# Kernel optimization log

Measured on AMD Instinct MI355X. Metric: run time of the kernel, lower is better.

## Reference

```python
import jax, jax.numpy as jnp
import numpy as np

N = 50000      # node_num
DIN = 128      # input_dim
DH = 128       # hidden_dim
DE = 128       # embedding_dim
DD = 128       # decoder_dim
NE = 800000    # num edges (before self loops)
B = 4096       # drug pairs
EPS = 1e-5


def setup_inputs() -> dict:
    key = jax.random.key(0)
    ks = jax.random.split(key, 16)
    x = jax.random.normal(ks[0], (N, DIN), jnp.float32)
    edge_index = jax.random.randint(ks[1], (2, NE), 0, N, dtype=jnp.int32)
    drug_index = jax.random.randint(ks[2], (B, 2), 0, N, dtype=jnp.int32)
    s = 0.05  # weight scale for numerical sanity
    return {
        "x": x,
        "edge_index": edge_index,
        "drug_index": drug_index,
        "w1": jax.random.normal(ks[3], (DIN, DH), jnp.float32) * s,
        "b1": jnp.zeros((DH,), jnp.float32),
        "w2": jax.random.normal(ks[4], (DH, DH), jnp.float32) * s,
        "b2": jnp.zeros((DH,), jnp.float32),
        "w3": jax.random.normal(ks[5], (DH, DE), jnp.float32) * s,
        "b3": jnp.zeros((DE,), jnp.float32),
        "g1": jnp.ones((DH,), jnp.float32), "be1": jnp.zeros((DH,), jnp.float32),
        "g2": jnp.ones((DH,), jnp.float32), "be2": jnp.zeros((DH,), jnp.float32),
        "g3": jnp.ones((DE,), jnp.float32), "be3": jnp.zeros((DE,), jnp.float32),
        "p1": jax.random.normal(ks[6], (DE, DD), jnp.float32) * s,
        "p2": jax.random.normal(ks[7], (DD, DD), jnp.float32) * s,
    }


def gcn_conv(x, row, col, W, b):
    # row/col already include self loops; PyG: message from row (source), aggregated at col (target)
    n = x.shape[0]
    h = x @ W + b                                   # linear first, as in GCNConv.forward
    deg = jnp.zeros((n,), h.dtype).at[col].add(1.0)  # degree(col) incl. self loops -> >= 1
    dis = deg ** -0.5
    norm = dis[row] * dis[col]                      # [E+N]
    msg = norm[:, None] * h[row]                    # [E+N, d] gather
    return jax.ops.segment_sum(msg, col, num_segments=n)  # scatter-add


def batch_norm(x, gamma, beta):
    m = jnp.mean(x, axis=0)
    v = jnp.mean((x - m) ** 2, axis=0)  # biased var, as torch BatchNorm training
    return (x - m) * jax.lax.rsqrt(v + EPS) * gamma + beta


def leaky(x):
    return jnp.where(x >= 0, x, 0.1 * x)  # LeakyReLU(0.1)


def reference(x, edge_index, drug_index, w1, b1, w2, b2, w3, b3,
              g1, be1, g2, be2, g3, be3, p1, p2):
    n = x.shape[0]
    self_loop = jnp.arange(n, dtype=edge_index.dtype)
    row = jnp.concatenate([edge_index[0], self_loop])
    col = jnp.concatenate([edge_index[1], self_loop])

    h = leaky(batch_norm(gcn_conv(x, row, col, w1, b1), g1, be1))
    h = leaky(batch_norm(gcn_conv(h, row, col, w2, b2), g2, be2))
    h = leaky(batch_norm(gcn_conv(h, row, col, w3, b3), g3, be3))

    di = drug_index.reshape(-1, 2)
    a = h[di[:, 0] - 1]  # [B, DE] (1-based indices; -1 wraps like torch negative index)
    bb = h[di[:, 1] - 1]  # [B, DE]
    t = a @ p1 @ p2 @ p1.T            # [B, DE] bilinear decode, batched
    ypred = jnp.sum(t * bb, axis=1, keepdims=True)  # [B, 1]
    return ypred
```

## Files before the change

### kernel.cpp

```cpp
#include <hip/hip_runtime.h>

#define PAD 64
#define NSLOT 64

__global__ void init_kernel(int* __restrict__ cnt, float* __restrict__ stats, int n, int nstat) {
  int i = blockIdx.x * blockDim.x + threadIdx.x;
  int stride = gridDim.x * blockDim.x;
  for (int j = i; j < n; j += stride) cnt[j] = 0;
  for (int j = i; j < nstat; j += stride) stats[j] = 0.f;
}

__global__ void fillcsr_kernel(const int* __restrict__ row, const int* __restrict__ col,
                               int* __restrict__ cnt, int* __restrict__ csr, int ne) {
  int e = blockIdx.x * blockDim.x + threadIdx.x;
  if (e < ne) {
    int d = col[e];
    int p = atomicAdd(&cnt[d], 1);
    if (p < PAD) csr[d * PAD + p] = row[e];
  }
}

__global__ __launch_bounds__(256) void gemm_kernel(
    const float* __restrict__ A, const float* __restrict__ W, const float* __restrict__ bias,
    float* __restrict__ out, int n, float invN,
    const float* __restrict__ bn_sum, const float* __restrict__ bn_sq,
    const float* __restrict__ bn_g, const float* __restrict__ bn_b, int use_bn,
    const int* __restrict__ cnt) {
  __shared__ float Ws[128 * 128];
  __shared__ float xs[128 * 128];
  __shared__ float bnsc[128], bnsh[128];
  int tid = threadIdx.x;
  if (tid < 128) {
    if (use_bn) {
      float s = 0.f, q = 0.f;
      for (int r2 = 0; r2 < NSLOT; ++r2) { s += bn_sum[r2 * 128 + tid]; q += bn_sq[r2 * 128 + tid]; }
      float m = s * invN;
      float var = q * invN - m * m;
      float rs = rsqrtf(var + 1e-5f);
      float sc = rs * bn_g[tid];
      bnsc[tid] = sc;
      bnsh[tid] = bn_b[tid] - m * sc;
    } else {
      bnsc[tid] = 1.f; bnsh[tid] = 0.f;
    }
  }
  const float4* W4 = (const float4*)W;
  float4* Ws4 = (float4*)Ws;
#pragma unroll
  for (int m = 0; m < 16; ++m) Ws4[tid + m * 256] = W4[tid + m * 256];
  __syncthreads();
  int base = blockIdx.x * 128;
  {
    int hf = tid >> 7;
    int r = tid & 127;
    int row = base + r;
    const float4* Arow = (const float4*)(A + (size_t)row * 128);
#pragma unroll
    for (int m = 0; m < 16; ++m) {
      int kblk = 2 * m + hf;
      int k0 = kblk * 4;
      float4 v = make_float4(0.f, 0.f, 0.f, 0.f);
      if (row < n) v = Arow[kblk];
      if (use_bn) {
        float t;
        t = v.x * bnsc[k0 + 0] + bnsh[k0 + 0]; v.x = t >= 0.f ? t : 0.1f * t;
        t = v.y * bnsc[k0 + 1] + bnsh[k0 + 1]; v.y = t >= 0.f ? t : 0.1f * t;
        t = v.z * bnsc[k0 + 2] + bnsh[k0 + 2]; v.z = t >= 0.f ? t : 0.1f * t;
        t = v.w * bnsc[k0 + 3] + bnsh[k0 + 3]; v.w = t >= 0.f ? t : 0.1f * t;
      }
      xs[(k0 + 0) * 128 + r] = v.x;
      xs[(k0 + 1) * 128 + r] = v.y;
      xs[(k0 + 2) * 128 + r] = v.z;
      xs[(k0 + 3) * 128 + r] = v.w;
    }
  }
  __syncthreads();
  int tx = tid & 15, ty = tid >> 4;
  int c0 = tx * 4, r0 = ty * 4;
  float acc[8][8];
#pragma unroll
  for (int i = 0; i < 8; ++i)
#pragma unroll
    for (int j = 0; j < 8; ++j) acc[i][j] = 0.f;
#pragma unroll 4
  for (int k = 0; k < 128; ++k) {
    float4 a0 = *(const float4*)&xs[k * 128 + r0];
    float4 a1 = *(const float4*)&xs[k * 128 + 64 + r0];
    float4 w0 = *(const float4*)&Ws[k * 128 + c0];
    float4 w1 = *(const float4*)&Ws[k * 128 + 64 + c0];
    float xr[8], wc[8];
    xr[0] = a0.x; xr[1] = a0.y; xr[2] = a0.z; xr[3] = a0.w;
    xr[4] = a1.x; xr[5] = a1.y; xr[6] = a1.z; xr[7] = a1.w;
    wc[0] = w0.x; wc[1] = w0.y; wc[2] = w0.z; wc[3] = w0.w;
    wc[4] = w1.x; wc[5] = w1.y; wc[6] = w1.z; wc[7] = w1.w;
#pragma unroll
    for (int i = 0; i < 8; ++i)
#pragma unroll
      for (int j = 0; j < 8; ++j)
        acc[i][j] = fmaf(xr[i], wc[j], acc[i][j]);
  }
  float bb0[4], bb1[4];
#pragma unroll
  for (int j = 0; j < 4; ++j) { bb0[j] = bias[c0 + j]; bb1[j] = bias[64 + c0 + j]; }
#pragma unroll
  for (int i = 0; i < 8; ++i) {
    int row = base + (i < 4 ? r0 + i : 64 + r0 + (i - 4));
    if (row < n) {
      float rs = rsqrtf((float)(cnt[row] + 1));
      float4 o0, o1;
      o0.x = (acc[i][0] + bb0[0]) * rs; o0.y = (acc[i][1] + bb0[1]) * rs;
      o0.z = (acc[i][2] + bb0[2]) * rs; o0.w = (acc[i][3] + bb0[3]) * rs;
      o1.x = (acc[i][4] + bb1[0]) * rs; o1.y = (acc[i][5] + bb1[1]) * rs;
      o1.z = (acc[i][6] + bb1[2]) * rs; o1.w = (acc[i][7] + bb1[3]) * rs;
      *(float4*)&out[(size_t)row * 128 + c0] = o0;
      *(float4*)&out[(size_t)row * 128 + 64 + c0] = o1;
    }
  }
}

__global__ __launch_bounds__(256) void agg_kernel(const float* __restrict__ z,
                                                  const int* __restrict__ cnt,
                                                  const int* __restrict__ csr,
                                                  float* __restrict__ out,
                                                  float* __restrict__ Ssum,
                                                  float* __restrict__ Ssq,
                                                  int n, int half) {
  __shared__ float bs[4][128], bq[4][128];
  int tid = threadIdx.x;
  int lane = tid & 63;
  int wv = tid >> 6;
  int w = (blockIdx.x * blockDim.x + tid) >> 6;
  float stx = 0.f, sty = 0.f, qtx = 0.f, qty = 0.f;
  if (w < half) {
    int i0 = w, i1 = w + half;
    bool has1 = (i1 < n);
    const float2* __restrict__ h2 = (const float2*)z;
    unsigned off0 = (unsigned)i0 * 64u + (unsigned)lane;
    unsigned off1 = (unsigned)i1 * 64u + (unsigned)lane;
    float2 self0 = h2[off0];
    float2 self1 = has1 ? h2[off1] : make_float2(0.f, 0.f);
    int c0r = cnt[i0];
    int c1r = has1 ? cnt[i1] : 0;
    float d0 = rsqrtf((float)(c0r + 1));
    float d1 = rsqrtf((float)(c1r + 1));
    int e0 = c0r > PAD ? PAD : c0r;
    int e1 = c1r > PAD ? PAD : c1r;
    const int* __restrict__ lp0 = csr + (size_t)i0 * PAD;
    const int* __restrict__ lp1 = csr + (size_t)i1 * PAD;
    float s0x = self0.x, s0y = self0.y;
    float s1x = self1.x, s1y = self1.y;
    int my0 = (lane < e0) ? lp0[lane] : 0;
    int my1 = (lane < e1) ? lp1[lane] : 0;
    int p0 = 0, p1 = 0;
    while (p0 + 8 <= e0 && p1 + 8 <= e1) {
      float2 v0[8], v1[8];
#pragma unroll
      for (int u = 0; u < 8; ++u) { int s = __shfl(my0, p0 + u, 64); v0[u] = h2[(unsigned)s * 64u + (unsigned)lane]; }
#pragma unroll
      for (int u = 0; u < 8; ++u) { int s = __shfl(my1, p1 + u, 64); v1[u] = h2[(unsigned)s * 64u + (unsigned)lane]; }
#pragma unroll
      for (int u = 0; u < 8; ++u) {
        s0x += v0[u].x; s0y += v0[u].y;
        s1x += v1[u].x; s1y += v1[u].y;
      }
      p0 += 8; p1 += 8;
    }
    for (; p0 + 8 <= e0; p0 += 8) {
      float2 v[8];
#pragma unroll
      for (int u = 0; u < 8; ++u) { int s = __shfl(my0, p0 + u, 64); v[u] = h2[(unsigned)s * 64u + (unsigned)lane]; }
#pragma unroll
      for (int u = 0; u < 8; ++u) { s0x += v[u].x; s0y += v[u].y; }
    }
    for (; p0 + 4 <= e0; p0 += 4) {
      float2 v[4];
#pragma unroll
      for (int u = 0; u < 4; ++u) { int s = __shfl(my0, p0 + u, 64); v[u] = h2[(unsigned)s * 64u + (unsigned)lane]; }
#pragma unroll
      for (int u = 0; u < 4; ++u) { s0x += v[u].x; s0y += v[u].y; }
    }
    for (; p0 < e0; ++p0) {
      int s = __shfl(my0, p0, 64);
      float2 v = h2[(unsigned)s * 64u + (unsigned)lane];
      s0x += v.x; s0y += v.y;
    }
    for (; p1 + 8 <= e1; p1 += 8) {
      float2 v[8];
#pragma unroll
      for (int u = 0; u < 8; ++u) { int s = __shfl(my1, p1 + u, 64); v[u] = h2[(unsigned)s * 64u + (unsigned)lane]; }
#pragma unroll
      for (int u = 0; u < 8; ++u) { s1x += v[u].x; s1y += v[u].y; }
    }
    for (; p1 + 4 <= e1; p1 += 4) {
      float2 v[4];
#pragma unroll
      for (int u = 0; u < 4; ++u) { int s = __shfl(my1, p1 + u, 64); v[u] = h2[(unsigned)s * 64u + (unsigned)lane]; }
#pragma unroll
      for (int u = 0; u < 4; ++u) { s1x += v[u].x; s1y += v[u].y; }
    }
    for (; p1 < e1; ++p1) {
      int s = __shfl(my1, p1, 64);
      float2 v = h2[(unsigned)s * 64u + (unsigned)lane];
      s1x += v.x; s1y += v.y;
    }
    float2 o0; o0.x = d0 * s0x; o0.y = d0 * s0y;
    ((float2*)out)[off0] = o0;
    stx += o0.x; qtx = fmaf(o0.x, o0.x, qtx);
    sty += o0.y; qty = fmaf(o0.y, o0.y, qty);
    if (has1) {
      float2 o1; o1.x = d1 * s1x; o1.y = d1 * s1y;
      ((float2*)out)[off1] = o1;
      stx += o1.x; qtx = fmaf(o1.x, o1.x, qtx);
      sty += o1.y; qty = fmaf(o1.y, o1.y, qty);
    }
  }
  bs[wv][2 * lane] = stx;     bs[wv][2 * lane + 1] = sty;
  bq[wv][2 * lane] = qtx;     bq[wv][2 * lane + 1] = qty;
  __syncthreads();
  if (tid < 128) {
    float s = bs[0][tid] + bs[1][tid] + bs[2][tid] + bs[3][tid];
    float q = bq[0][tid] + bq[1][tid] + bq[2][tid] + bq[3][tid];
    int slot = (blockIdx.x & (NSLOT - 1)) * 128 + tid;
    atomicAdd(&Ssum[slot], s);
    atomicAdd(&Ssq[slot], q);
  }
}

__global__ __launch_bounds__(128) void mm128_kernel(const float* __restrict__ A, const float* __restrict__ B,
                                                    float* __restrict__ C, int transB) {
  __shared__ float Ar[128];
  int i = blockIdx.x, j = threadIdx.x;
  Ar[j] = A[i * 128 + j];
  __syncthreads();
  float acc = 0.f;
  if (transB) {
    for (int k = 0; k < 128; ++k) acc = fmaf(Ar[k], B[j * 128 + k], acc);
  } else {
    for (int k = 0; k < 128; ++k) acc = fmaf(Ar[k], B[k * 128 + j], acc);
  }
  C[i * 128 + j] = acc;
}

__global__ __launch_bounds__(256) void decoder_kernel(
    const float* __restrict__ h, const int* __restrict__ di, const float* __restrict__ M,
    const float* __restrict__ bn_sum, const float* __restrict__ bn_sq,
    const float* __restrict__ bn_g, const float* __restrict__ bn_b,
    float* __restrict__ out, int npairs, int n, float invN) {
  __shared__ float Ms[128 * 128];
  __shared__ float sc[128], sh[128];
  int tid = threadIdx.x;
  if (tid < 128) {
    float s = 0.f, q = 0.f;
    for (int r2 = 0; r2 < NSLOT; ++r2) { s += bn_sum[r2 * 128 + tid]; q += bn_sq[r2 * 128 + tid]; }
    float m = s * invN;
    float var = q * invN - m * m;
    float rs = rsqrtf(var + 1e-5f);
    float scv = rs * bn_g[tid];
    sc[tid] = scv;
    sh[tid] = bn_b[tid] - m * scv;
  }
  for (int t = tid; t < 4096; t += 256) ((float4*)Ms)[t] = ((const float4*)M)[t];
  __syncthreads();
  int lane = tid & 63, wv = tid >> 6;
  int wid = blockIdx.x * 4 + wv;
  int nw = gridDim.x * 4;
  for (int k = wid; k < npairs; k += nw) {
    int ia = di[2 * k] - 1;     if (ia < 0) ia += n;
    int ib = di[2 * k + 1] - 1; if (ib < 0) ib += n;
    const float* ap = h + (size_t)ia * 128;
    const float* bp = h + (size_t)ib * 128;
    float u0 = 0.f, u1 = 0.f;
#pragma unroll 8
    for (int i = 0; i < 128; ++i) {
      float av = ap[i] * sc[i] + sh[i];
      av = av >= 0.f ? av : 0.1f * av;
      u0 = fmaf(av, Ms[i * 128 + lane], u0);
      u1 = fmaf(av, Ms[i * 128 + 64 + lane], u1);
    }
    float b0 = bp[lane] * sc[lane] + sh[lane];            b0 = b0 >= 0.f ? b0 : 0.1f * b0;
    float b1 = bp[lane + 64] * sc[lane + 64] + sh[lane + 64]; b1 = b1 >= 0.f ? b1 : 0.1f * b1;
    float part = u0 * b0 + u1 * b1;
#pragma unroll
    for (int o = 32; o; o >>= 1) part += __shfl_down(part, o, 64);
    if (lane == 0) out[k] = part;
  }
}

extern "C" void kernel_launch(void* const* d_in, const int* in_sizes, int n_in,
                              void* d_out, int out_size, void* d_ws, size_t ws_size,
                              hipStream_t stream) {
  const float* x   = (const float*)d_in[0];
  const int*   ei  = (const int*)d_in[1];
  const int*   dri = (const int*)d_in[2];
  const float* w1  = (const float*)d_in[3];
  const float* b1  = (const float*)d_in[4];
  const float* w2  = (const float*)d_in[5];
  const float* b2  = (const float*)d_in[6];
  const float* w3  = (const float*)d_in[7];
  const float* b3  = (const float*)d_in[8];
  const float* g1  = (const float*)d_in[9];
  const float* be1 = (const float*)d_in[10];
  const float* g2  = (const float*)d_in[11];
  const float* be2 = (const float*)d_in[12];
  const float* g3  = (const float*)d_in[13];
  const float* be3 = (const float*)d_in[14];
  const float* p1  = (const float*)d_in[15];
  const float* p2  = (const float*)d_in[16];
  float* out = (float*)d_out;

  int n  = in_sizes[0] / 128;
  int ne = in_sizes[1] / 2;
  int np = in_sizes[2] / 2;
  const int* erow = ei;
  const int* ecol = ei + ne;

  size_t o = 0;
  char* wsb = (char*)d_ws;
  auto alloc = [&](size_t bytes) { void* p = wsb + o; o += (bytes + 255) & ~255ull; return p; };
  float* T1   = (float*)alloc((size_t)n * 128 * 4);
  float* T2   = (float*)alloc((size_t)n * 128 * 4);
  int*   csr  = (int*)alloc((size_t)n * PAD * 4);
  int*   cnt  = (int*)alloc((size_t)n * 4);
  int nstat = 6 * NSLOT * 128;
  float* stats = (float*)alloc((size_t)nstat * 4);
  float* M1   = (float*)alloc(128 * 128 * 4);
  float* M2   = (float*)alloc(128 * 128 * 4);
  float* Ssum1 = stats;
  float* Ssq1  = stats + 1 * NSLOT * 128;
  float* Ssum2 = stats + 2 * NSLOT * 128;
  float* Ssq2  = stats + 3 * NSLOT * 128;
  float* Ssum3 = stats + 4 * NSLOT * 128;
  float* Ssq3  = stats + 5 * NSLOT * 128;

  float invN = 1.0f / (float)n;
  int eb = (ne + 255) / 256;
  int gb = (n + 127) / 128;
  int half = (n + 1) / 2;
  int ab = (half + 3) / 4;

  init_kernel<<<512, 256, 0, stream>>>(cnt, stats, n, nstat);
  fillcsr_kernel<<<eb, 256, 0, stream>>>(erow, ecol, cnt, csr, ne);

  gemm_kernel<<<gb, 256, 0, stream>>>(x, w1, b1, T1, n, invN, nullptr, nullptr, nullptr, nullptr, 0, cnt);
  agg_kernel<<<ab, 256, 0, stream>>>(T1, cnt, csr, T2, Ssum1, Ssq1, n, half);

  gemm_kernel<<<gb, 256, 0, stream>>>(T2, w2, b2, T1, n, invN, Ssum1, Ssq1, g1, be1, 1, cnt);
  agg_kernel<<<ab, 256, 0, stream>>>(T1, cnt, csr, T2, Ssum2, Ssq2, n, half);

  gemm_kernel<<<gb, 256, 0, stream>>>(T2, w3, b3, T1, n, invN, Ssum2, Ssq2, g2, be2, 1, cnt);
  agg_kernel<<<ab, 256, 0, stream>>>(T1, cnt, csr, T2, Ssum3, Ssq3, n, half);

  mm128_kernel<<<128, 128, 0, stream>>>(p1, p2, M1, 0);
  mm128_kernel<<<128, 128, 0, stream>>>(M1, p1, M2, 1);
  decoder_kernel<<<256, 256, 0, stream>>>(T2, dri, M2, Ssum3, Ssq3, g3, be3, out, np, n, invN);
}
```

Measured before the change: 398.3 us.

## Split GEMM K dimension into 32-wide shared-memory chunks to raise occupancy

```diff
diff --git a/kernel.cpp b/kernel.cpp
--- a/kernel.cpp
+++ b/kernel.cpp
@@ -20,14 +20,14 @@
   }
 }
 
-__global__ __launch_bounds__(256) void gemm_kernel(
+__global__ __launch_bounds__(256, 4) void gemm_kernel(
     const float* __restrict__ A, const float* __restrict__ W, const float* __restrict__ bias,
     float* __restrict__ out, int n, float invN,
     const float* __restrict__ bn_sum, const float* __restrict__ bn_sq,
     const float* __restrict__ bn_g, const float* __restrict__ bn_b, int use_bn,
     const int* __restrict__ cnt) {
-  __shared__ float Ws[128 * 128];
-  __shared__ float xs[128 * 128];
+  __shared__ float Ws[32 * 128];
+  __shared__ float xs[32 * 128];
   __shared__ float bnsc[128], bnsh[128];
   int tid = threadIdx.x;
   if (tid < 128) {
@@ -44,60 +44,66 @@
       bnsc[tid] = 1.f; bnsh[tid] = 0.f;
     }
   }
-  const float4* W4 = (const float4*)W;
-  float4* Ws4 = (float4*)Ws;
-#pragma unroll
-  for (int m = 0; m < 16; ++m) Ws4[tid + m * 256] = W4[tid + m * 256];
-  __syncthreads();
   int base = blockIdx.x * 128;
-  {
-    int hf = tid >> 7;
-    int r = tid & 127;
-    int row = base + r;
-    const float4* Arow = (const float4*)(A + (size_t)row * 128);
-#pragma unroll
-    for (int m = 0; m < 16; ++m) {
-      int kblk = 2 * m + hf;
-      int k0 = kblk * 4;
+  int tx = tid & 15, ty = tid >> 4;
+  int c0 = tx * 4, r0 = ty * 4;
+  int r = tid & 127;
+  int row_s = base + r;
+  int hf = tid >> 7;
+  int kw = tid >> 5;
+  int c4 = tid & 31;
+  const float4* Arow = (const float4*)(A + (size_t)row_s * 128);
+  float acc[8][8];
+#pragma unroll
+  for (int i = 0; i < 8; ++i)
+#pragma unroll
+    for (int j = 0; j < 8; ++j) acc[i][j] = 0.f;
+
+  for (int kp = 0; kp < 4; ++kp) {
+    __syncthreads();
+#pragma unroll
+    for (int it = 0; it < 4; ++it) {
+      int kl = kw + it * 8;
+      float4 wv = ((const float4*)(W + (size_t)(kp * 32 + kl) * 128))[c4];
+      *(float4*)&Ws[kl * 128 + c4 * 4] = wv;
+    }
+#pragma unroll
+    for (int it = 0; it < 4; ++it) {
+      int kbl = hf + it * 2;
       float4 v = make_float4(0.f, 0.f, 0.f, 0.f);
-      if (row < n) v = Arow[kblk];
+      if (row_s < n) v = Arow[kp * 8 + kbl];
       if (use_bn) {
+        int k0 = kp * 32 + kbl * 4;
         float t;
         t = v.x * bnsc[k0 + 0] + bnsh[k0 + 0]; v.x = t >= 0.f ? t : 0.1f * t;
         t = v.y * bnsc[k0 + 1] + bnsh[k0 + 1]; v.y = t >= 0.f ? t : 0.1f * t;
         t = v.z * bnsc[k0 + 2] + bnsh[k0 + 2]; v.z = t >= 0.f ? t : 0.1f * t;
         t = v.w * bnsc[k0 + 3] + bnsh[k0 + 3]; v.w = t >= 0.f ? t : 0.1f * t;
       }
-      xs[(k0 + 0) * 128 + r] = v.x;
-      xs[(k0 + 1) * 128 + r] = v.y;
-      xs[(k0 + 2) * 128 + r] = v.z;
-      xs[(k0 + 3) * 128 + r] = v.w;
-    }
-  }
-  __syncthreads();
-  int tx = tid & 15, ty = tid >> 4;
-  int c0 = tx * 4, r0 = ty * 4;
-  float acc[8][8];
-#pragma unroll
-  for (int i = 0; i < 8; ++i)
-#pragma unroll
-    for (int j = 0; j < 8; ++j) acc[i][j] = 0.f;
+      int kl = kbl * 4;
+      xs[(kl + 0) * 128 + r] = v.x;
+      xs[(kl + 1) * 128 + r] = v.y;
+      xs[(kl + 2) * 128 + r] = v.z;
+      xs[(kl + 3) * 128 + r] = v.w;
+    }
+    __syncthreads();
 #pragma unroll 4
-  for (int k = 0; k < 128; ++k) {
-    float4 a0 = *(const float4*)&xs[k * 128 + r0];
-    float4 a1 = *(const float4*)&xs[k * 128 + 64 + r0];
-    float4 w0 = *(const float4*)&Ws[k * 128 + c0];
-    float4 w1 = *(const float4*)&Ws[k * 128 + 64 + c0];
-    float xr[8], wc[8];
-    xr[0] = a0.x; xr[1] = a0.y; xr[2] = a0.z; xr[3] = a0.w;
-    xr[4] = a1.x; xr[5] = a1.y; xr[6] = a1.z; xr[7] = a1.w;
-    wc[0] = w0.x; wc[1] = w0.y; wc[2] = w0.z; wc[3] = w0.w;
-    wc[4] = w1.x; wc[5] = w1.y; wc[6] = w1.z; wc[7] = w1.w;
-#pragma unroll
-    for (int i = 0; i < 8; ++i)
-#pragma unroll
-      for (int j = 0; j < 8; ++j)
-        acc[i][j] = fmaf(xr[i], wc[j], acc[i][j]);
+    for (int k = 0; k < 32; ++k) {
+      float4 a0 = *(const float4*)&xs[k * 128 + r0];
+      float4 a1 = *(const float4*)&xs[k * 128 + 64 + r0];
+      float4 w0 = *(const float4*)&Ws[k * 128 + c0];
+      float4 w1 = *(const float4*)&Ws[k * 128 + 64 + c0];
+      float xr[8], wc[8];
+      xr[0] = a0.x; xr[1] = a0.y; xr[2] = a0.z; xr[3] = a0.w;
+      xr[4] = a1.x; xr[5] = a1.y; xr[6] = a1.z; xr[7] = a1.w;
+      wc[0] = w0.x; wc[1] = w0.y; wc[2] = w0.z; wc[3] = w0.w;
+      wc[4] = w1.x; wc[5] = w1.y; wc[6] = w1.z; wc[7] = w1.w;
+#pragma unroll
+      for (int i = 0; i < 8; ++i)
+#pragma unroll
+        for (int j = 0; j < 8; ++j)
+          acc[i][j] = fmaf(xr[i], wc[j], acc[i][j]);
+    }
   }
   float bb0[4], bb1[4];
 #pragma unroll
```

New measurement: 383.4 us. 1.04x faster.
